# Kernel tuning notes

Hardware: AMD Instinct MI355X
Metric: run time of the kernel (lower is better)

The kernel has to match this reference:

```python
import jax, jax.numpy as jnp
import numpy as np

N = 131072   # queries
M = 8192     # tree nodes
K = 8        # max children per node
DEPTH = 16   # upper bound on traversal depth (complete 8-ary tree of 8192 nodes has depth ~5)
EPS = 1e-6   # torch PairwiseDistance eps (added to the difference)
BIG = 1e9    # finite stand-in for +inf so grads stay clean


def _mlp(x, W1, b1, W2, b2, W3, b3, W4, b4):
    # TransformNetwork: 2 -> 100 -> 100 -> 30 -> 2, ReLU on hidden layers
    h = jax.nn.relu(x @ W1 + b1)
    h = jax.nn.relu(h @ W2 + b2)
    h = jax.nn.relu(h @ W3 + b3)
    return h @ W4 + b4


def setup_inputs() -> dict:
    key = jax.random.key(0)
    ks = jax.random.split(key, 8)
    x = jax.random.normal(ks[0], (N, 2), dtype=jnp.float32)
    node_data = jax.random.normal(ks[1], (M, 2), dtype=jnp.float32)
    rng = np.random.default_rng(0)
    node_classes = jnp.asarray(np.eye(2, dtype=np.float32)[rng.integers(0, 2, M)])
    # complete K-ary tree: parent of node i (i>=1) is (i-1)//K
    ch = np.full((M, K), -1, dtype=np.int32)
    idx = np.arange(1, M)
    ch[(idx - 1) // K, (idx - 1) % K] = idx
    children = jnp.asarray(ch)
    W1 = jax.random.normal(ks[2], (2, 100), dtype=jnp.float32) * 0.7
    W2 = jax.random.normal(ks[3], (100, 100), dtype=jnp.float32) * 0.1
    W3 = jax.random.normal(ks[4], (100, 30), dtype=jnp.float32) * 0.1
    W4 = jax.random.normal(ks[5], (30, 2), dtype=jnp.float32) * 0.18
    b1 = jnp.zeros((100,), jnp.float32)
    b2 = jnp.zeros((100,), jnp.float32)
    b3 = jnp.zeros((30,), jnp.float32)
    b4 = jnp.zeros((2,), jnp.float32)
    return {"x": x, "node_data": node_data, "node_classes": node_classes,
            "children": children, "W1": W1, "b1": b1, "W2": W2, "b2": b2,
            "W3": W3, "b3": b3, "W4": W4, "b4": b4}


def _forward(x, node_data, node_classes, children, W1, b1, W2, b2, W3, b3, W4, b4):
    emb = _mlp(node_data, W1, b1, W2, b2, W3, b3, W4, b4)   # [M,2] transformed node data
    qx = _mlp(x, W1, b1, W2, b2, W3, b3, W4, b4)            # [N,2] transformed queries
    valid = children >= 0                                    # [M,K]
    ch = jnp.where(valid, children, 0)                       # safe gather indices

    def dist(a, b):
        # torch.nn.PairwiseDistance: ||a - b + eps||_2
        return jnp.sqrt(jnp.sum((a - b + EPS) ** 2, axis=-1))

    def traverse(q):
        def step(carry, t):
            cur, prob, done, out = carry
            c_idx = ch[cur]                    # [K]
            c_val = valid[cur]                 # [K]
            c_emb = emb[c_idx]                 # [K,2]
            d0 = dist(emb[cur], q)             # scalar: current node
            dc = jnp.where(c_val, dist(c_emb, q), BIG)          # [K] children (pad -> BIG)
            all_d = jnp.concatenate([d0[None], dc])             # [K+1]
            logp = jax.nn.log_softmax(-all_d)
            max_prob = jnp.max(logp)
            amax = jnp.argmax(logp)
            # quirk in source: first iteration adds max_prob twice (prob = max_prob; prob += max_prob)
            prob_new = prob + max_prob + jnp.where(t == 0, max_prob, 0.0)
            stop = amax == 0
            # prob2: log of softmax(-child-to-current distances)-weighted class mixture
            d2 = jnp.where(c_val, dist(emb[cur], c_emb), BIG)    # [K]
            w = jax.nn.softmax(-d2)                              # pad weights ~0
            mix = w @ (node_classes[c_idx] * c_val[:, None].astype(q.dtype))  # [2]
            prob2 = jnp.log(jnp.maximum(mix, 1e-30))
            has_child = jnp.any(c_val)
            out_stop = jnp.where(has_child, prob_new + prob2, jnp.full((2,), prob_new))
            new_out = jnp.where(done, out, jnp.where(stop, out_stop, out))
            nxt = ch[cur][jnp.maximum(amax - 1, 0)]
            new_cur = jnp.where(done | stop, cur, nxt)
            new_prob = jnp.where(done, prob, prob_new)
            return (new_cur, new_prob, done | stop, new_out), None

        init = (jnp.int32(0), jnp.float32(0.0), jnp.array(False), jnp.zeros((2,), q.dtype))
        (_, _, _, out), _ = jax.lax.scan(step, init, jnp.arange(DEPTH))
        return out

    return jax.vmap(traverse)(qx)   # [N,2]


def reference(x, node_data, node_classes, children, W1, b1, W2, b2, W3, b3, W4, b4):
    return _forward(x, node_data, node_classes, children, W1, b1, W2, b2, W3, b3, W4, b4)
```

## Files before the change

kernel.cpp:

```cpp
#include <hip/hip_runtime.h>
#include <math.h>

#define NQ 131072
#define MN 8192
#define NINT 1024
#define DEPTHT 16
#define EPSD 1e-6f
#define BIGD 1e9f

__global__ __launch_bounds__(256) void transpose_w2(
    const float* __restrict__ W2, float* __restrict__ W2T)
{
    const int i = blockIdx.x * 256 + threadIdx.x;
    if (i < 100 * 100) {
        const int k = i / 100, j = i - k * 100;
        W2T[j * 100 + k] = W2[i];
    }
}

__global__ __launch_bounds__(64, 2) void mlp_kernel(
    const float* __restrict__ x, const float* __restrict__ nd,
    const float* __restrict__ W1, const float* __restrict__ b1,
    const float* __restrict__ W2T, const float* __restrict__ b2,
    const float* __restrict__ W3, const float* __restrict__ b3,
    const float* __restrict__ W4, const float* __restrict__ b4,
    float* __restrict__ outv)
{
    const int r = blockIdx.x * 64 + threadIdx.x;
    const float2 xi = (r < NQ) ? ((const float2*)x)[r]
                               : ((const float2*)nd)[r - NQ];

    float h1[100];
#pragma unroll
    for (int k = 0; k < 100; ++k)
        h1[k] = fmaxf(fmaf(xi.x, W1[k], fmaf(xi.y, W1[100 + k], b1[k])), 0.0f);

    float h3[30];
#pragma unroll
    for (int jj = 0; jj < 30; ++jj) h3[jj] = b3[jj];

    const float* w2 = W2T;
    const float* w3 = W3;
    for (int j = 0; j < 100; ++j) {
        float a0 = 0.0f, a1 = 0.0f;
#pragma unroll
        for (int k = 0; k < 100; k += 2) {
            a0 = fmaf(h1[k],     w2[k],     a0);
            a1 = fmaf(h1[k + 1], w2[k + 1], a1);
        }
        const float h2j = fmaxf(a0 + a1 + b2[j], 0.0f);
#pragma unroll
        for (int jj = 0; jj < 30; ++jj)
            h3[jj] = fmaf(h2j, w3[jj], h3[jj]);
        w2 += 100;
        w3 += 30;
    }

    float o0 = b4[0], o1 = b4[1];
#pragma unroll
    for (int k = 0; k < 30; ++k) {
        const float h = fmaxf(h3[k], 0.0f);
        o0 = fmaf(h, W4[2 * k],     o0);
        o1 = fmaf(h, W4[2 * k + 1], o1);
    }
    ((float2*)outv)[r] = make_float2(o0, o1);
}

__global__ __launch_bounds__(256) void prob2_kernel(
    const float2* __restrict__ emb, const float2* __restrict__ cls,
    float2* __restrict__ p2)
{
    const int i = blockIdx.x * 256 + threadIdx.x;
    const float2 ei = emb[i];
    const int base = 8 * i + 1;

    float d2[8];
    float m2 = BIGD;
#pragma unroll
    for (int j = 0; j < 8; ++j) {
        const int c = base + j;
        const bool v = c < MN;
        const float2 ec = emb[v ? c : 0];
        const float dx = ei.x - ec.x + EPSD;
        const float dy = ei.y - ec.y + EPSD;
        d2[j] = v ? sqrtf(dx * dx + dy * dy) : BIGD;
        m2 = fminf(m2, d2[j]);
    }
    float s2 = 0.0f, mix0 = 0.0f, mix1 = 0.0f;
#pragma unroll
    for (int j = 0; j < 8; ++j) {
        const float w = expf(m2 - d2[j]);
        s2 += w;
        const int c = base + j;
        if (c < MN) {
            const float2 cv = cls[c];
            mix0 = fmaf(w, cv.x, mix0);
            mix1 = fmaf(w, cv.y, mix1);
        }
    }
    mix0 /= s2;
    mix1 /= s2;
    p2[i] = make_float2(logf(fmaxf(mix0, 1e-30f)),
                        logf(fmaxf(mix1, 1e-30f)));
}

__global__ __launch_bounds__(256) void traverse_kernel(
    const float* __restrict__ qx, const float2* __restrict__ emb,
    const float2* __restrict__ p2g, float* __restrict__ out)
{
    __shared__ float2 semb[MN];
    __shared__ float2 sp2[NINT];
    {
        const float4* ge = (const float4*)emb;
        float4* se = (float4*)semb;
#pragma unroll
        for (int t = 0; t < 16; ++t)
            se[threadIdx.x + 256 * t] = ge[threadIdx.x + 256 * t];
        const float4* gp = (const float4*)p2g;
        float4* sp = (float4*)sp2;
#pragma unroll
        for (int t = 0; t < 2; ++t)
            sp[threadIdx.x + 256 * t] = gp[threadIdx.x + 256 * t];
    }
    __syncthreads();

    const int qi = blockIdx.x * 256 + threadIdx.x;
    const float2 qv = ((const float2*)qx)[qi];

    int cur = 0;
    float d0;
    {
        const float2 e0 = semb[0];
        const float dx = e0.x - qv.x + EPSD;
        const float dy = e0.y - qv.y + EPSD;
        d0 = sqrtf(dx * dx + dy * dy);
    }
    float prob = 0.0f, out0 = 0.0f, out1 = 0.0f;
    bool done = false;

    for (int t = 0; t < DEPTHT; ++t) {
        if (__all(done)) break;
        if (!done) {
            const int base = 8 * cur + 1;

            float dc[8];
#pragma unroll
            for (int j = 0; j < 8; ++j) {
                const int c = base + j;
                const bool v = c < MN;
                const float2 e = semb[v ? c : 0];
                const float dx = e.x - qv.x + EPSD;
                const float dy = e.y - qv.y + EPSD;
                dc[j] = v ? sqrtf(dx * dx + dy * dy) : BIGD;
            }

            float dmin = d0;
            int amax = 0;
#pragma unroll
            for (int j = 0; j < 8; ++j)
                if (dc[j] < dmin) { dmin = dc[j]; amax = j + 1; }

            float s = expf(dmin - d0);
#pragma unroll
            for (int j = 0; j < 8; ++j) s += expf(dmin - dc[j]);
            const float max_prob = -logf(s);
            const float prob_new = prob + max_prob + ((t == 0) ? max_prob : 0.0f);

            if (amax == 0) {
                if (base < MN) {
                    const float2 pp = sp2[cur];
                    out0 = prob_new + pp.x;
                    out1 = prob_new + pp.y;
                } else {
                    out0 = prob_new;
                    out1 = prob_new;
                }
                done = true;
            } else {
                cur  = base + amax - 1;
                d0   = dmin;
                prob = prob_new;
            }
        }
    }

    ((float2*)out)[qi] = make_float2(out0, out1);
}

extern "C" void kernel_launch(void* const* d_in, const int* in_sizes, int n_in,
                              void* d_out, int out_size, void* d_ws, size_t ws_size,
                              hipStream_t stream)
{
    const float* x   = (const float*)d_in[0];
    const float* nd  = (const float*)d_in[1];
    const float* cls = (const float*)d_in[2];
    const float* W1 = (const float*)d_in[4];
    const float* b1 = (const float*)d_in[5];
    const float* W2 = (const float*)d_in[6];
    const float* b2 = (const float*)d_in[7];
    const float* W3 = (const float*)d_in[8];
    const float* b3 = (const float*)d_in[9];
    const float* W4 = (const float*)d_in[10];
    const float* b4 = (const float*)d_in[11];

    float* ws   = (float*)d_ws;
    float* qx   = ws;
    float* embf = ws + 2 * NQ;
    float* p2f  = ws + 2 * (NQ + MN);
    float* w2t  = p2f + 2 * NINT;

    transpose_w2<<<40, 256, 0, stream>>>(W2, w2t);

    mlp_kernel<<<(NQ + MN) / 64, 64, 0, stream>>>(
        x, nd, W1, b1, w2t, b2, W3, b3, W4, b4, qx);

    prob2_kernel<<<NINT / 256, 256, 0, stream>>>(
        (const float2*)embf, (const float2*)cls, (float2*)p2f);

    traverse_kernel<<<NQ / 256, 256, 0, stream>>>(
        qx, (const float2*)embf, (const float2*)p2f, (float*)d_out);
}
```

Measured before the change: 156.6 us.

## Fuse prob2 into traversal and read embeddings from global instead of LDS

Removes the separate prob2 kernel launch and computes the stop-node class mixture inline inside the traversal kernel when a query stops. The traversal kernel also stops staging the 64KB embedding table into shared memory and reads it directly from global memory (cached in L1/L2). This removes a launch and the per-block LDS fill and barrier. In exchange, each stopping thread recomputes the prob2 work and pays global-memory gather latency on every child lookup.

Measured after the change: 159.9 us. 2.1% more time.

```diff
diff --git a/kernel.cpp b/kernel.cpp
--- a/kernel.cpp
+++ b/kernel.cpp
@@ -7,6 +7,7 @@
 #define DEPTHT 16
 #define EPSD 1e-6f
 #define BIGD 1e9f
+
 
 __global__ __launch_bounds__(256) void transpose_w2(
     const float* __restrict__ W2, float* __restrict__ W2T)
@@ -66,71 +67,17 @@
     ((float2*)outv)[r] = make_float2(o0, o1);
 }
 
-__global__ __launch_bounds__(256) void prob2_kernel(
-    const float2* __restrict__ emb, const float2* __restrict__ cls,
-    float2* __restrict__ p2)
-{
-    const int i = blockIdx.x * 256 + threadIdx.x;
-    const float2 ei = emb[i];
-    const int base = 8 * i + 1;
-
-    float d2[8];
-    float m2 = BIGD;
-#pragma unroll
-    for (int j = 0; j < 8; ++j) {
-        const int c = base + j;
-        const bool v = c < MN;
-        const float2 ec = emb[v ? c : 0];
-        const float dx = ei.x - ec.x + EPSD;
-        const float dy = ei.y - ec.y + EPSD;
-        d2[j] = v ? sqrtf(dx * dx + dy * dy) : BIGD;
-        m2 = fminf(m2, d2[j]);
-    }
-    float s2 = 0.0f, mix0 = 0.0f, mix1 = 0.0f;
-#pragma unroll
-    for (int j = 0; j < 8; ++j) {
-        const float w = expf(m2 - d2[j]);
-        s2 += w;
-        const int c = base + j;
-        if (c < MN) {
-            const float2 cv = cls[c];
-            mix0 = fmaf(w, cv.x, mix0);
-            mix1 = fmaf(w, cv.y, mix1);
-        }
-    }
-    mix0 /= s2;
-    mix1 /= s2;
-    p2[i] = make_float2(logf(fmaxf(mix0, 1e-30f)),
-                        logf(fmaxf(mix1, 1e-30f)));
-}
-
 __global__ __launch_bounds__(256) void traverse_kernel(
     const float* __restrict__ qx, const float2* __restrict__ emb,
-    const float2* __restrict__ p2g, float* __restrict__ out)
+    const float2* __restrict__ cls, float* __restrict__ out)
 {
-    __shared__ float2 semb[MN];
-    __shared__ float2 sp2[NINT];
-    {
-        const float4* ge = (const float4*)emb;
-        float4* se = (float4*)semb;
-#pragma unroll
-        for (int t = 0; t < 16; ++t)
-            se[threadIdx.x + 256 * t] = ge[threadIdx.x + 256 * t];
-        const float4* gp = (const float4*)p2g;
-        float4* sp = (float4*)sp2;
-#pragma unroll
-        for (int t = 0; t < 2; ++t)
-            sp[threadIdx.x + 256 * t] = gp[threadIdx.x + 256 * t];
-    }
-    __syncthreads();
-
     const int qi = blockIdx.x * 256 + threadIdx.x;
     const float2 qv = ((const float2*)qx)[qi];
 
     int cur = 0;
     float d0;
     {
-        const float2 e0 = semb[0];
+        const float2 e0 = emb[0];
         const float dx = e0.x - qv.x + EPSD;
         const float dy = e0.y - qv.y + EPSD;
         d0 = sqrtf(dx * dx + dy * dy);
@@ -148,7 +95,7 @@
             for (int j = 0; j < 8; ++j) {
                 const int c = base + j;
                 const bool v = c < MN;
-                const float2 e = semb[v ? c : 0];
+                const float2 e = emb[v ? c : 0];
                 const float dx = e.x - qv.x + EPSD;
                 const float dy = e.y - qv.y + EPSD;
                 dc[j] = v ? sqrtf(dx * dx + dy * dy) : BIGD;
@@ -168,9 +115,35 @@
 
             if (amax == 0) {
                 if (base < MN) {
-                    const float2 pp = sp2[cur];
-                    out0 = prob_new + pp.x;
-                    out1 = prob_new + pp.y;
+                    const float2 ei = emb[cur];
+                    float d2[8];
+                    float m2 = BIGD;
+#pragma unroll
+                    for (int j = 0; j < 8; ++j) {
+                        const int c = base + j;
+                        const bool v = c < MN;
+                        const float2 ec = emb[v ? c : 0];
+                        const float dx = ei.x - ec.x + EPSD;
+                        const float dy = ei.y - ec.y + EPSD;
+                        d2[j] = v ? sqrtf(dx * dx + dy * dy) : BIGD;
+                        m2 = fminf(m2, d2[j]);
+                    }
+                    float s2 = 0.0f, mix0 = 0.0f, mix1 = 0.0f;
+#pragma unroll
+                    for (int j = 0; j < 8; ++j) {
+                        const float w = expf(m2 - d2[j]);
+                        s2 += w;
+                        const int c = base + j;
+                        if (c < MN) {
+                            const float2 cv = cls[c];
+                            mix0 = fmaf(w, cv.x, mix0);
+                            mix1 = fmaf(w, cv.y, mix1);
+                        }
+                    }
+                    mix0 /= s2;
+                    mix1 /= s2;
+                    out0 = prob_new + logf(fmaxf(mix0, 1e-30f));
+                    out1 = prob_new + logf(fmaxf(mix1, 1e-30f));
                 } else {
                     out0 = prob_new;
                     out1 = prob_new;
@@ -206,17 +179,13 @@
     float* ws   = (float*)d_ws;
     float* qx   = ws;
     float* embf = ws + 2 * NQ;
-    float* p2f  = ws + 2 * (NQ + MN);
-    float* w2t  = p2f + 2 * NINT;
+    float* w2t  = ws + 2 * (NQ + MN);
 
     transpose_w2<<<40, 256, 0, stream>>>(W2, w2t);
 
     mlp_kernel<<<(NQ + MN) / 64, 64, 0, stream>>>(
         x, nd, W1, b1, w2t, b2, W3, b3, W4, b4, qx);
 
-    prob2_kernel<<<NINT / 256, 256, 0, stream>>>(
-        (const float2*)embf, (const float2*)cls, (float2*)p2f);
-
     traverse_kernel<<<NQ / 256, 256, 0, stream>>>(
-        qx, (const float2*)embf, (const float2*)p2f, (float*)d_out);
+        qx, (const float2*)embf, (const float2*)cls, (float*)d_out);
 }
```
